# Optimization experiments

Hardware: AMD Instinct MI355X
Metric: run time of the kernel (lower is better)

## Reference

```python
import jax, jax.numpy as jnp
import numpy as np

# ---- config (matches init_kwargs) ----
GROUP_NUM = 2048
K_NEIGHBORS = 32
OUT_DIM = 192
SIGMA, BASELINE, SCALING, EPS = 0.26, 0.1, 10.0, 1e-6
ALPHA, BETA = 1000.0, 100.0
ADAPTIVE_RATIO = 0.5
IN_DIM = 3
ADAPTIVE_DIM = int(OUT_DIM * ADAPTIVE_RATIO)          # 96
FOURIER_DIM = OUT_DIM - ADAPTIVE_DIM                  # 96
FEAT_DIM_F = FOURIER_DIM // (IN_DIM * 2)              # 16
FEAT_DIM_A = int(np.ceil(ADAPTIVE_DIM / IN_DIM))      # 32
FEAT_NUM_A = FEAT_DIM_A * IN_DIM                      # 96
OUT_IDX = np.linspace(0, FEAT_NUM_A - 1, ADAPTIVE_DIM).astype(np.int64)


def setup_inputs() -> dict:
    key = jax.random.key(0)
    k1, k2, k3, k4 = jax.random.split(key, 4)
    xyz = jax.random.normal(k1, (4, 8192, 3), dtype=jnp.float32)
    x = jax.random.normal(k2, (4, 8192, 96), dtype=jnp.float32)
    bn_gamma = jax.random.uniform(k3, (192,), dtype=jnp.float32)
    bn_beta = jax.random.normal(k4, (192,), dtype=jnp.float32)
    return {"xyz": xyz, "x": x, "bn_gamma": bn_gamma, "bn_beta": bn_beta}


def _fps(xyz, m):
    """Farthest point sampling. xyz: [B,N,3] -> idx [B,m] (int32). Seed = index 0."""
    def single(pts):
        n = pts.shape[0]
        def step(carry, _):
            dists, last = carry
            d = jnp.sum((pts - pts[last]) ** 2, axis=-1)
            dists = jnp.minimum(dists, d)
            nxt = jnp.argmax(dists).astype(jnp.int32)
            return (dists, nxt), nxt
        init = (jnp.full((n,), 1e10, pts.dtype), jnp.array(0, jnp.int32))
        _, idxs = jax.lax.scan(step, init, None, length=m - 1)
        return jnp.concatenate([jnp.zeros((1,), jnp.int32), idxs])
    return jax.vmap(single)(xyz)


def _square_distance(src, dst):
    # src: [B,S,3], dst: [B,N,3] -> [B,S,N]
    d = -2.0 * jnp.einsum('bsc,bnc->bsn', src, dst)
    d += jnp.sum(src ** 2, -1)[:, :, None]
    d += jnp.sum(dst ** 2, -1)[:, None, :]
    return d


def _gather_knn(points, idx):
    # points: [B,N,C], idx: [B,G,K] -> [B,G,K,C]
    return jax.vmap(lambda p, i: p[i])(points, idx)


def _forward(xyz, x, bn_gamma, bn_beta):
    B, N, _ = xyz.shape
    G, K = GROUP_NUM, K_NEIGHBORS

    # ---- Grouper_seg ----
    fps_idx = _fps(xyz, G)                                   # [B,G]
    lc_xyz = jnp.take_along_axis(xyz, fps_idx[..., None], 1)  # [B,G,3]
    lc_x = jnp.take_along_axis(x, fps_idx[..., None], 1)      # [B,G,C]
    sqr = _square_distance(lc_xyz, xyz)                       # [B,G,N]
    knn_idx = jax.lax.top_k(-sqr, K)[1]                       # [B,G,K] smallest-k
    knn_xyz = _gather_knn(xyz, knn_idx)                       # [B,G,K,3]
    knn_x = _gather_knn(x, knn_idx)                           # [B,G,K,C]

    # ---- Aggregation_seg: local normalization ----
    mean_x = lc_x[:, :, None, :]
    std_x = jnp.std(knn_x - mean_x, ddof=1)
    mean_xyz = lc_xyz[:, :, None, :]
    std_xyz = jnp.std(knn_xyz - mean_xyz, ddof=1)
    knn_x = (knn_x - mean_x) / (std_x + 1e-5)
    knn_xyz_n = (knn_xyz - mean_xyz) / (std_xyz + 1e-5)       # [B,G,K,3]
    C = knn_x.shape[-1]
    knn_x = jnp.concatenate(
        [knn_x, jnp.broadcast_to(lc_x[:, :, None, :], (B, G, K, C))], axis=-1)  # [B,G,K,2C]
    knn_xyz_cf = jnp.transpose(knn_xyz_n, (0, 3, 1, 2))       # [B,3,G,K]
    knn_x_cf = jnp.transpose(knn_x, (0, 3, 1, 2))             # [B,OUT_DIM,G,K]

    # ---- PosE_Geo: fourier part ----
    feat_range = jnp.arange(FEAT_DIM_F, dtype=knn_xyz_cf.dtype)
    dim_embed = ALPHA ** (feat_range / FEAT_DIM_F)            # [F]
    div = BETA * knn_xyz_cf[..., None] / dim_embed            # [B,3,G,K,F]
    fourier = jnp.stack([jnp.sin(div), jnp.cos(div)], axis=-1)  # [B,3,G,K,F,2]
    fourier = fourier.reshape(B, IN_DIM, G, K, 2 * FEAT_DIM_F)
    fourier = jnp.transpose(fourier, (0, 1, 4, 2, 3)).reshape(B, FOURIER_DIM, G, K)

    # ---- AdaptiveEmbedding (parameterless, data-driven) ----
    x4 = knn_xyz_n                                            # [B,G,K,3]
    gstd = jnp.mean(jnp.std(x4.reshape(B, -1, IN_DIM), axis=1, ddof=1))
    sig = SIGMA * (1.0 + gstd) + EPS
    blend = jax.nn.sigmoid((gstd - BASELINE) * SCALING)
    feat_val = jnp.linspace(-1.0, 1.0, FEAT_DIM_A + 2)[1:-1]  # [Fa]
    z = (x4[..., None] - feat_val) / sig                      # [B,G,K,3,Fa]
    comb = blend * jnp.exp(-0.5 * z * z) + (1.0 - blend) * jnp.cos(z)
    ae = comb.reshape(B, G, K, FEAT_NUM_A)[..., OUT_IDX]      # [B,G,K,ADAPTIVE_DIM]
    ae_cf = jnp.transpose(ae, (0, 3, 1, 2))                   # [B,ADAPTIVE_DIM,G,K]

    pe = jnp.concatenate([fourier, ae_cf], axis=1)            # [B,OUT_DIM,G,K]
    knn_x_w = (knn_x_cf + pe) * pe

    # ---- Pooling_seg: max+mean pool, BatchNorm1d (train stats) + GELU ----
    lc = jnp.max(knn_x_w, -1) + jnp.mean(knn_x_w, -1)         # [B,OUT_DIM,G]
    mu = jnp.mean(lc, axis=(0, 2), keepdims=True)
    var = jnp.var(lc, axis=(0, 2), keepdims=True)
    y = (lc - mu) / jnp.sqrt(var + 1e-5)
    y = y * bn_gamma[None, :, None] + bn_beta[None, :, None]
    return jax.nn.gelu(y, approximate=False)


def reference(xyz, x, bn_gamma, bn_beta):
    return _forward(xyz, x, bn_gamma, bn_beta)
```

## Files before the change

kernel.cpp:

```cpp
#include <hip/hip_runtime.h>
#include <cstdint>
#include <math.h>

#define NPTS 8192
#define NB 4
#define NG 2048
#define NK 32
#define CIN 96
#define COUT 192

typedef float v2f __attribute__((ext_vector_type(2)));
typedef unsigned long long ull;

__global__ __launch_bounds__(256) void setup_kernel(const float* __restrict__ xyz,
                                                    float* __restrict__ xs, float* __restrict__ ys,
                                                    float* __restrict__ zs, float* __restrict__ d2){
  int i = blockIdx.x*256 + threadIdx.x;
  if (i >= NB*NPTS) return;
  float x = xyz[3*i+0], y = xyz[3*i+1], z = xyz[3*i+2];
  xs[i]=x; ys[i]=y; zs[i]=z;
  d2[i] = __fadd_rn(__fadd_rn(__fmul_rn(x,x),__fmul_rn(y,y)),__fmul_rn(z,z));
}

template<int CTRL>
__device__ __forceinline__ float dppmaxf(float v){
  int o = __builtin_amdgcn_update_dpp(__float_as_int(v), __float_as_int(v), CTRL, 0xf, 0xf, false);
  return fmaxf(v, __int_as_float(o));
}
template<int CTRL>
__device__ __forceinline__ unsigned dppminu(unsigned v){
  unsigned o = (unsigned)__builtin_amdgcn_update_dpp((int)v, (int)v, CTRL, 0xf, 0xf, false);
  return (o < v) ? o : v;
}
__device__ __forceinline__ float wavemaxf(float v){
  v = dppmaxf<0x111>(v); v = dppmaxf<0x112>(v); v = dppmaxf<0x114>(v);
  v = dppmaxf<0x118>(v); v = dppmaxf<0x142>(v); v = dppmaxf<0x143>(v);
  return v;
}
__device__ __forceinline__ unsigned waveminu(unsigned v){
  v = dppminu<0x111>(v); v = dppminu<0x112>(v); v = dppminu<0x114>(v);
  v = dppminu<0x118>(v); v = dppminu<0x142>(v); v = dppminu<0x143>(v);
  return v;
}

__global__ __launch_bounds__(512,2) void fps_kernel(const float* __restrict__ xyz, int* __restrict__ fps_idx){
#pragma clang fp contract(off)
  extern __shared__ char smem[];
  float4* ctab = (float4*)smem;
  ull* wavekeys = (ull*)(smem + NPTS*16);
  const int b = blockIdx.x;
  const int t = threadIdx.x;
  const int w = t>>6, lane = t&63;
  const float* base = xyz + (size_t)b*NPTS*3;
  v2f px[8], py[8], pz[8], D[8];
#pragma unroll
  for (int j=0;j<8;++j){
    int p0 = t + 1024*j, p1 = p0 + 512;
    float x0=base[3*p0+0], y0=base[3*p0+1], z0=base[3*p0+2];
    float x1=base[3*p1+0], y1=base[3*p1+1], z1=base[3*p1+2];
    px[j]=(v2f){x0,x1}; py[j]=(v2f){y0,y1}; pz[j]=(v2f){z0,z1};
    D[j]=(v2f){1e10f,1e10f};
    ctab[p0] = make_float4(x0,y0,z0,0.f);
    ctab[p1] = make_float4(x1,y1,z1,0.f);
  }
  if (t==0) fps_idx[b*NG]=0;
  __syncthreads();
  float lx=base[0], ly=base[1], lz=base[2];
  for (int it=0; it<NG-1; ++it){
    v2f bm = (v2f){-1.0f,-1.0f};
#pragma unroll
    for (int j=0;j<8;++j){
      v2f dx = px[j]-lx, dy = py[j]-ly, dz = pz[j]-lz;
      v2f s = (dx*dx + dy*dy) + dz*dz;
      v2f nd = __builtin_elementwise_min(D[j], s);
      D[j] = nd;
      bm = __builtin_elementwise_max(bm, nd);
    }
    float bd = fmaxf(bm.x, bm.y);
    float m = wavemaxf(bd);
    float bdw = __int_as_float(__builtin_amdgcn_readlane(__float_as_int(m), 63));
    unsigned li = 0xFFFFFFFFu;
    if (bd == bdw){
#pragma unroll
      for (int j=7;j>=0;--j){
        if (D[j].y == bdw) li = (unsigned)(t + (j<<10) + 512);
        if (D[j].x == bdw) li = (unsigned)(t + (j<<10));
      }
    }
    unsigned mn = waveminu(li);
    if (lane==63)
      wavekeys[(it&1)*8 + w] = (((ull)__float_as_uint(bdw))<<32) | (ull)(~mn);
    __syncthreads();
    const ull* wk = wavekeys + (it&1)*8;
    ull k = wk[0];
#pragma unroll
    for (int q=1;q<8;++q){ ull o = wk[q]; if (o > k) k = o; }
    unsigned pw = ~(unsigned)k;
    float4 c = ctab[pw];
    lx=c.x; ly=c.y; lz=c.z;
    if (t==0) fps_idx[b*NG + it + 1] = (int)pw;
  }
}

__device__ __forceinline__ bool lexlt(float ad, int ai, float bd, int bi){
  return (ad < bd) || ((ad == bd) && (ai < bi));
}
__device__ __forceinline__ void sort_desc(float& d, int& i, int lane){
#pragma unroll
  for (int k=2;k<=64;k<<=1){
#pragma unroll
    for (int j=k>>1;j>0;j>>=1){
      float od = __shfl_xor(d, j);
      int   oi = __shfl_xor(i, j);
      bool dirUp = (lane & k) != 0;
      bool lower = (lane & j) == 0;
      bool less  = lexlt(d,i,od,oi);
      bool keep  = (less == (lower == dirUp));
      if (!keep){ d=od; i=oi; }
    }
  }
}
__device__ __forceinline__ void merge_asc(float& d, int& i, int lane){
#pragma unroll
  for (int j=32;j>0;j>>=1){
    float od = __shfl_xor(d, j);
    int   oi = __shfl_xor(i, j);
    bool lower = (lane & j) == 0;
    bool less  = lexlt(d,i,od,oi);
    bool keep  = (less == lower);
    if (!keep){ d=od; i=oi; }
  }
}

__global__ __launch_bounds__(256) void knn_kernel(const float* __restrict__ xs, const float* __restrict__ ys,
                                                  const float* __restrict__ zs, const float* __restrict__ d2,
                                                  const int* __restrict__ fps_idx, int* __restrict__ knn_out){
  __shared__ float tx[256], ty[256], tz[256], td[256];
  const int tid = threadIdx.x;
  const int wid = tid>>6, lane = tid&63;
  const int pid = blockIdx.x*4 + wid;
  const int b = pid >> 11;
  const float* bx = xs + b*NPTS;
  const float* by = ys + b*NPTS;
  const float* bz = zs + b*NPTS;
  const float* bD = d2 + b*NPTS;
  const int fi = fps_idx[pid];
  const float ax = bx[fi], ay = by[fi], az = bz[fi];
  const float src2 = __fadd_rn(__fadd_rn(__fmul_rn(ax,ax),__fmul_rn(ay,ay)),__fmul_rn(az,az));
  float Ad = INFINITY; int Ai = 0x7fffffff;
  float tau_d = INFINITY; int tau_i = 0x7fffffff;
  for (int s=0; s<NPTS/256; ++s){
    __syncthreads();
    int gidx = s*256 + tid;
    tx[tid]=bx[gidx]; ty[tid]=by[gidx]; tz[tid]=bz[gidx]; td[tid]=bD[gidx];
    __syncthreads();
    float m0,m1,m2,m3; int i0,i1,i2,i3;
#define LOADJ(mj, ij, J) { int li = (J)*64 + lane; \
    float dot = __fadd_rn(__fadd_rn(__fmul_rn(ax,tx[li]),__fmul_rn(ay,ty[li])),__fmul_rn(az,tz[li])); \
    mj = __fadd_rn(__fadd_rn(__fmul_rn(-2.0f,dot), src2), td[li]); ij = s*256 + li; }
    LOADJ(m0,i0,0) LOADJ(m1,i1,1) LOADJ(m2,i2,2) LOADJ(m3,i3,3)
#undef LOADJ
    while (true){
      bool any = lexlt(m0,i0,tau_d,tau_i) || lexlt(m1,i1,tau_d,tau_i) ||
                 lexlt(m2,i2,tau_d,tau_i) || lexlt(m3,i3,tau_d,tau_i);
      if (__ballot(any) == 0ull) break;
      float cd = m0; int ci = i0; int sel = 0;
      if (lexlt(m1,i1,cd,ci)){ cd=m1; ci=i1; sel=1; }
      if (lexlt(m2,i2,cd,ci)){ cd=m2; ci=i2; sel=2; }
      if (lexlt(m3,i3,cd,ci)){ cd=m3; ci=i3; sel=3; }
      if      (sel==0) m0=INFINITY;
      else if (sel==1) m1=INFINITY;
      else if (sel==2) m2=INFINITY;
      else             m3=INFINITY;
      sort_desc(cd, ci, lane);
      if (lexlt(cd,ci,Ad,Ai)){ Ad=cd; Ai=ci; }
      merge_asc(Ad, Ai, lane);
      tau_d = __shfl(Ad, 31);
      tau_i = __shfl(Ai, 31);
    }
  }
  if (lane < NK) knn_out[pid*NK + lane] = Ai;
}

__global__ __launch_bounds__(256) void stats_kernel(const float* __restrict__ x, const float* __restrict__ xyz,
                                                    const int* __restrict__ fps_idx, const int* __restrict__ knn,
                                                    double* __restrict__ partials){
  const int tid=threadIdx.x, wid=tid>>6, lane=tid&63;
  const int pid = blockIdx.x*4 + wid;
  const int b = pid>>11;
  const int fi = fps_idx[pid];
  const float* xb = x + (size_t)b*NPTS*CIN;
  const float* zb = xyz + (size_t)b*NPTS*3;
  const float lc0 = xb[fi*CIN + lane];
  float lc1 = 0.f; if (lane<32) lc1 = xb[fi*CIN + 64 + lane];
  float czv = 0.f; if (lane<3)  czv = zb[fi*3 + lane];
  double s1=0.0, s2=0.0, a1=0.0, a2=0.0;
  for (int k=0;k<NK;++k){
    int idx = knn[pid*NK + k];
    float d0 = __fsub_rn(xb[idx*CIN + lane], lc0);
    s1 += (double)d0; s2 += (double)d0*(double)d0;
    if (lane<32){
      float d1 = __fsub_rn(xb[idx*CIN + 64 + lane], lc1);
      s1 += (double)d1; s2 += (double)d1*(double)d1;
    }
    if (lane<3){
      float w = __fsub_rn(zb[idx*3 + lane], czv);
      a1 += (double)w; a2 += (double)w*(double)w;
    }
  }
#pragma unroll
  for (int off=32; off>0; off>>=1){ s1 += __shfl_xor(s1,off); s2 += __shfl_xor(s2,off); }
  __shared__ double shx[4][2];
  __shared__ double shz[4][3][2];
  if (lane==0){ shx[wid][0]=s1; shx[wid][1]=s2; }
  if (lane<3){ shz[wid][lane][0]=a1; shz[wid][lane][1]=a2; }
  __syncthreads();
  if (tid==0){
    double u0=0,u1=0;
    for (int w=0;w<4;++w){ u0+=shx[w][0]; u1+=shx[w][1]; }
    double* outp = partials + (size_t)blockIdx.x*8;
    outp[0]=u0; outp[1]=u1;
    for (int axq=0; axq<3; ++axq){
      double v0=0,v1=0;
      for (int w=0;w<4;++w){ v0+=shz[w][axq][0]; v1+=shz[w][axq][1]; }
      outp[2+2*axq]=v0; outp[3+2*axq]=v1;
    }
  }
}

__global__ void finalize_kernel(const double* __restrict__ partials, float* __restrict__ scal){
  const int lane = threadIdx.x;
  double s1=0,s2=0;
  double z0a=0,z0b=0,z1a=0,z1b=0,z2a=0,z2b=0;
  for (int i=0;i<32;++i){
    const double* p = partials + (size_t)(lane*32+i)*8;
    s1+=p[0]; s2+=p[1];
    z0a+=p[2]; z0b+=p[3]; z1a+=p[4]; z1b+=p[5]; z2a+=p[6]; z2b+=p[7];
  }
#pragma unroll
  for (int off=32; off>0; off>>=1){ s1+=__shfl_xor(s1,off); s2+=__shfl_xor(s2,off); }
#pragma unroll
  for (int off=8; off>0; off>>=1){
    z0a+=__shfl_xor(z0a,off); z0b+=__shfl_xor(z0b,off);
    z1a+=__shfl_xor(z1a,off); z1b+=__shfl_xor(z1b,off);
    z2a+=__shfl_xor(z2a,off); z2b+=__shfl_xor(z2b,off);
  }
  __shared__ double zb[4][3][2];
  if ((lane&15)==0){
    int b = lane>>4;
    zb[b][0][0]=z0a; zb[b][0][1]=z0b;
    zb[b][1][0]=z1a; zb[b][1][1]=z1b;
    zb[b][2][0]=z2a; zb[b][2][1]=z2b;
  }
  __syncthreads();
  if (lane==0){
    double nx = (double)NB*NG*NK*CIN;
    double varx = (s2 - s1*s1/nx)/(nx-1.0);
    float stdx = (float)sqrt(varx);
    double t1=0,t2=0;
    for (int b=0;b<4;++b) for (int a=0;a<3;++a){ t1+=zb[b][a][0]; t2+=zb[b][a][1]; }
    double nz = (double)NB*NG*NK*3;
    double varz = (t2 - t1*t1/nz)/(nz-1.0);
    float stdz = (float)sqrt(varz);
    float sdiv = stdz + 1e-5f;
    double n2 = (double)NG*NK;
    double acc=0.0;
    for (int b=0;b<4;++b) for (int a=0;a<3;++a){
      double v = (zb[b][a][1] - zb[b][a][0]*zb[b][a][0]/n2)/(n2-1.0);
      acc += sqrt(v);
    }
    float gstd = (float)(acc/12.0) / sdiv;
    float sig = 0.26f*(1.0f+gstd) + 1e-6f;
    float blend = 1.0f/(1.0f + expf(-(gstd-0.1f)*10.0f));
    scal[0] = 1.0f/(stdx + 1e-5f);
    scal[1] = 1.0f/sdiv;
    scal[2] = 1.0f/sig;
    scal[3] = blend;
  }
}

__global__ __launch_bounds__(256) void main_kernel(const float* __restrict__ x, const float* __restrict__ xyz,
                                                   const int* __restrict__ fps_idx, const int* __restrict__ knn,
                                                   const float* __restrict__ scal, float* __restrict__ lc_out){
  const int tid=threadIdx.x, wid=tid>>6, lane=tid&63;
  const int pid = blockIdx.x*4 + wid;
  const int b = pid>>11, g = pid&2047;
  const float inv_x = scal[0], inv_z = scal[1], inv_sig = scal[2], blend = scal[3];
  const float omb = 1.0f - blend;
  const int fi = fps_idx[pid];
  const float* xb = x + (size_t)b*NPTS*CIN;
  const float* zb = xyz + (size_t)b*NPTS*3;
  const float cx = zb[fi*3+0], cy = zb[fi*3+1], cz = zb[fi*3+2];
  const float lcx0 = xb[fi*CIN + lane];
  const float lcx1 = (lane<32) ? xb[fi*CIN + 64 + lane] : xb[fi*CIN + lane - 32];
  const float lcx2 = xb[fi*CIN + 32 + lane];
  const int dim0 = lane>>5;
  const int rr0 = lane&31;
  const bool cos0 = rr0 & 1;
  const float bs0 = 100.0f / powf(1000.0f, (float)(rr0>>1) * (1.0f/16.0f));
  const bool cos1 = lane & 1;
  const float bs1 = 100.0f / powf(1000.0f, (float)((lane&31)>>1) * (1.0f/16.0f));
  const float fv1 = (float)(-1.0 + 2.0*(double)(lane-32+1)/33.0);
  const int dim2 = (32+lane)>>5;
  const int j2 = (32+lane)&31;
  const float fv2 = (float)(-1.0 + 2.0*(double)(j2+1)/33.0);

  float mx0=-INFINITY, mx1=-INFINITY, mx2=-INFINITY;
  float sm0=0.f, sm1=0.f, sm2=0.f;
  for (int k=0;k<NK;++k){
    const int idx = knn[pid*NK + k];
    const float p0 = zb[idx*3+0], p1 = zb[idx*3+1], p2v = zb[idx*3+2];
    const float xn0 = (p0-cx)*inv_z, xn1 = (p1-cy)*inv_z, xn2 = (p2v-cz)*inv_z;
    const float xk0 = xb[idx*CIN + lane];
    float xk1 = 0.f; if (lane<32) xk1 = xb[idx*CIN + 64 + lane];
    {
      float v = dim0 ? xn1 : xn0;
      float a = v * bs0;
      float pe = cos0 ? __cosf(a) : __sinf(a);
      float f = (xk0 - lcx0) * inv_x;
      float w = (f + pe) * pe;
      mx0 = fmaxf(mx0, w); sm0 += w;
    }
    {
      float pe, f;
      if (lane < 32){
        float a = xn2 * bs1;
        pe = cos1 ? __cosf(a) : __sinf(a);
        f = (xk1 - lcx1) * inv_x;
      } else {
        float zq = (xn0 - fv1) * inv_sig;
        pe = blend * __expf(-0.5f*zq*zq) + omb * __cosf(zq);
        f = lcx1;
      }
      float w = (f + pe) * pe;
      mx1 = fmaxf(mx1, w); sm1 += w;
    }
    {
      float v = (dim2==1) ? xn1 : xn2;
      float zq = (v - fv2) * inv_sig;
      float pe = blend * __expf(-0.5f*zq*zq) + omb * __cosf(zq);
      float w = (lcx2 + pe) * pe;
      mx2 = fmaxf(mx2, w); sm2 += w;
    }
  }
  const size_t obase = ((size_t)b*COUT)*NG + g;
  lc_out[obase + (size_t)lane*NG]       = mx0 + sm0*(1.0f/32.0f);
  lc_out[obase + (size_t)(64+lane)*NG]  = mx1 + sm1*(1.0f/32.0f);
  lc_out[obase + (size_t)(128+lane)*NG] = mx2 + sm2*(1.0f/32.0f);
}

__global__ __launch_bounds__(256) void bn_stats_kernel(const float* __restrict__ lc, float* __restrict__ bn){
  const int c = blockIdx.x, t = threadIdx.x, lane=t&63, wid=t>>6;
  double s1=0.0, s2=0.0;
  for (int i=t; i<NB*NG; i+=256){
    int b=i>>11, g=i&2047;
    float v = lc[((size_t)(b*COUT)+c)*NG + g];
    s1 += (double)v; s2 += (double)v*(double)v;
  }
#pragma unroll
  for (int off=32; off>0; off>>=1){ s1+=__shfl_xor(s1,off); s2+=__shfl_xor(s2,off); }
  __shared__ double sh1[4], sh2[4];
  if (lane==0){ sh1[wid]=s1; sh2[wid]=s2; }
  __syncthreads();
  if (t==0){
    double a=sh1[0]+sh1[1]+sh1[2]+sh1[3], q=sh2[0]+sh2[1]+sh2[2]+sh2[3];
    double n=(double)(NB*NG);
    double mu=a/n, var=q/n - mu*mu;
    bn[c]=(float)mu;
    bn[COUT+c]=(float)(1.0/sqrt(var + 1e-5));
  }
}

__global__ __launch_bounds__(256) void final_kernel(const float* __restrict__ bn, const float* __restrict__ gamma,
                                                    const float* __restrict__ beta, float* __restrict__ out){
  int i = blockIdx.x*256 + threadIdx.x;
  int c = (i >> 11) % COUT;
  float v = out[i];
  float y = (v - bn[c]) * bn[COUT + c];
  y = y*gamma[c] + beta[c];
  out[i] = y * 0.5f * (1.0f + erff(y * 0.70710678118654752f));
}

extern "C" void kernel_launch(void* const* d_in, const int* in_sizes, int n_in,
                              void* d_out, int out_size, void* d_ws, size_t ws_size,
                              hipStream_t stream){
  const float* xyz   = (const float*)d_in[0];
  const float* x     = (const float*)d_in[1];
  const float* gamma = (const float*)d_in[2];
  const float* beta  = (const float*)d_in[3];
  float* out = (float*)d_out;
  char* ws = (char*)d_ws;
  int*    fps  = (int*)   (ws + 0);
  int*    knn  = (int*)   (ws + 32768);
  float*  xs   = (float*) (ws + 1081344);
  float*  ys   = (float*) (ws + 1212416);
  float*  zs   = (float*) (ws + 1343488);
  float*  d2   = (float*) (ws + 1474560);
  double* parts= (double*)(ws + 1605632);
  float*  scal = (float*) (ws + 1736704);
  float*  bn   = (float*) (ws + 1736768);

  const int fps_lds = NPTS*16 + 2*8*8;
  (void)hipFuncSetAttribute(reinterpret_cast<const void*>(fps_kernel),
                            hipFuncAttributeMaxDynamicSharedMemorySize, fps_lds);

  setup_kernel   <<<dim3((NB*NPTS+255)/256), dim3(256), 0, stream>>>(xyz, xs, ys, zs, d2);
  fps_kernel     <<<dim3(NB),                dim3(512), fps_lds, stream>>>(xyz, fps);
  knn_kernel     <<<dim3(NB*NG/4),           dim3(256), 0, stream>>>(xs, ys, zs, d2, fps, knn);
  stats_kernel   <<<dim3(NB*NG/4),           dim3(256), 0, stream>>>(x, xyz, fps, knn, parts);
  finalize_kernel<<<dim3(1),                 dim3(64),  0, stream>>>(parts, scal);
  main_kernel    <<<dim3(NB*NG/4),           dim3(256), 0, stream>>>(x, xyz, fps, knn, scal, out);
  bn_stats_kernel<<<dim3(COUT),              dim3(256), 0, stream>>>(out, bn);
  final_kernel   <<<dim3((NB*COUT*NG)/256),  dim3(256), 0, stream>>>(bn, gamma, beta, out);
}
```

Measured before the change: 2.555 ms.

## Spatially sort FPS points per wave and skip waves via bounding-box bound

Reorders the points of each batch in the FPS kernel into Morton-ordered 8x8x8 cells, using a shared-memory histogram and scatter, so that each wave owns a spatially compact chunk with its own bounding box. At every iteration a wave computes a lower bound on the distance from the new centroid to its box. If that bound exceeds the wave's current max of min-distances, the wave skips the distance update and republishes its cached key. This is meant to remove most of the per-iteration distance work in the sequential FPS loop. The cost is setup work, extra registers (16 points per thread) and a key encoding that keeps the lowest-original-index tie-break.

```diff
diff --git a/kernel.cpp b/kernel.cpp
--- a/kernel.cpp
+++ b/kernel.cpp
@@ -9,7 +9,6 @@
 #define CIN 96
 #define COUT 192
 
-typedef float v2f __attribute__((ext_vector_type(2)));
 typedef unsigned long long ull;
 
 __global__ __launch_bounds__(256) void setup_kernel(const float* __restrict__ xyz,
@@ -28,18 +27,18 @@
   return fmaxf(v, __int_as_float(o));
 }
 template<int CTRL>
-__device__ __forceinline__ unsigned dppminu(unsigned v){
+__device__ __forceinline__ unsigned dppmaxu(unsigned v){
   unsigned o = (unsigned)__builtin_amdgcn_update_dpp((int)v, (int)v, CTRL, 0xf, 0xf, false);
-  return (o < v) ? o : v;
+  return (o > v) ? o : v;
 }
 __device__ __forceinline__ float wavemaxf(float v){
   v = dppmaxf<0x111>(v); v = dppmaxf<0x112>(v); v = dppmaxf<0x114>(v);
   v = dppmaxf<0x118>(v); v = dppmaxf<0x142>(v); v = dppmaxf<0x143>(v);
   return v;
 }
-__device__ __forceinline__ unsigned waveminu(unsigned v){
-  v = dppminu<0x111>(v); v = dppminu<0x112>(v); v = dppminu<0x114>(v);
-  v = dppminu<0x118>(v); v = dppminu<0x142>(v); v = dppminu<0x143>(v);
+__device__ __forceinline__ unsigned wavemaxu(unsigned v){
+  v = dppmaxu<0x111>(v); v = dppmaxu<0x112>(v); v = dppmaxu<0x114>(v);
+  v = dppmaxu<0x118>(v); v = dppmaxu<0x142>(v); v = dppmaxu<0x143>(v);
   return v;
 }
 
@@ -47,58 +46,141 @@
 #pragma clang fp contract(off)
   extern __shared__ char smem[];
   float4* ctab = (float4*)smem;
-  ull* wavekeys = (ull*)(smem + NPTS*16);
-  const int b = blockIdx.x;
-  const int t = threadIdx.x;
+  ull*    keys = (ull*)(smem + 131072);
+  int*    hist = (int*)(smem + 131072 + 128);
+  float*  bbs  = (float*)(smem + 131072 + 128 + 2048);
+  const int b = blockIdx.x, t = threadIdx.x;
   const int w = t>>6, lane = t&63;
   const float* base = xyz + (size_t)b*NPTS*3;
-  v2f px[8], py[8], pz[8], D[8];
-#pragma unroll
-  for (int j=0;j<8;++j){
-    int p0 = t + 1024*j, p1 = p0 + 512;
-    float x0=base[3*p0+0], y0=base[3*p0+1], z0=base[3*p0+2];
-    float x1=base[3*p1+0], y1=base[3*p1+1], z1=base[3*p1+2];
-    px[j]=(v2f){x0,x1}; py[j]=(v2f){y0,y1}; pz[j]=(v2f){z0,z1};
-    D[j]=(v2f){1e10f,1e10f};
-    ctab[p0] = make_float4(x0,y0,z0,0.f);
-    ctab[p1] = make_float4(x1,y1,z1,0.f);
-  }
-  if (t==0) fps_idx[b*NG]=0;
-  __syncthreads();
+
+  float ox[16], oy[16], oz[16];
+#pragma unroll
+  for (int j=0;j<16;++j){
+    int p = t + 512*j;
+    ox[j]=base[3*p+0]; oy[j]=base[3*p+1]; oz[j]=base[3*p+2];
+  }
+  float mnx=ox[0],mxx=ox[0],mny=oy[0],mxy=oy[0],mnz=oz[0],mxz=oz[0];
+#pragma unroll
+  for (int j=1;j<16;++j){
+    mnx=fminf(mnx,ox[j]); mxx=fmaxf(mxx,ox[j]);
+    mny=fminf(mny,oy[j]); mxy=fmaxf(mxy,oy[j]);
+    mnz=fminf(mnz,oz[j]); mxz=fmaxf(mxz,oz[j]);
+  }
+#pragma unroll
+  for (int off=32; off>0; off>>=1){
+    mnx=fminf(mnx,__shfl_xor(mnx,off)); mxx=fmaxf(mxx,__shfl_xor(mxx,off));
+    mny=fminf(mny,__shfl_xor(mny,off)); mxy=fmaxf(mxy,__shfl_xor(mxy,off));
+    mnz=fminf(mnz,__shfl_xor(mnz,off)); mxz=fmaxf(mxz,__shfl_xor(mxz,off));
+  }
+  hist[t] = 0;
+  if (lane==0){
+    bbs[w*6+0]=mnx; bbs[w*6+1]=mxx; bbs[w*6+2]=mny;
+    bbs[w*6+3]=mxy; bbs[w*6+4]=mnz; bbs[w*6+5]=mxz;
+  }
+  if (t==0) fps_idx[b*NG] = 0;
+  __syncthreads();
+  float gx0=1e30f,gx1=-1e30f,gy0=1e30f,gy1=-1e30f,gz0=1e30f,gz1=-1e30f;
+  for (int q=0;q<8;++q){
+    gx0=fminf(gx0,bbs[q*6+0]); gx1=fmaxf(gx1,bbs[q*6+1]);
+    gy0=fminf(gy0,bbs[q*6+2]); gy1=fmaxf(gy1,bbs[q*6+3]);
+    gz0=fminf(gz0,bbs[q*6+4]); gz1=fmaxf(gz1,bbs[q*6+5]);
+  }
+  const float sxv = 8.0f/fmaxf(gx1-gx0,1e-20f);
+  const float syv = 8.0f/fmaxf(gy1-gy0,1e-20f);
+  const float szv = 8.0f/fmaxf(gz1-gz0,1e-20f);
+  int cell[16];
+#pragma unroll
+  for (int j=0;j<16;++j){
+    int cx = min(7,(int)((ox[j]-gx0)*sxv));
+    int cy = min(7,(int)((oy[j]-gy0)*syv));
+    int cz = min(7,(int)((oz[j]-gz0)*szv));
+    int m = (cx&1) | ((cy&1)<<1) | ((cz&1)<<2)
+          | ((cx&2)<<2) | ((cy&2)<<3) | ((cz&2)<<4)
+          | ((cx&4)<<4) | ((cy&4)<<5) | ((cz&4)<<6);
+    cell[j]=m;
+    atomicAdd(&hist[m],1);
+  }
+  __syncthreads();
+  if (t==0){
+    int run=0;
+    for (int c=0;c<512;++c){ int h=hist[c]; hist[c]=run; run+=h; }
+  }
+  __syncthreads();
+#pragma unroll
+  for (int j=0;j<16;++j){
+    int pos = atomicAdd(&hist[cell[j]],1);
+    ctab[pos] = make_float4(ox[j],oy[j],oz[j], __int_as_float(t+512*j));
+  }
+  __syncthreads();
+  float px[16],py[16],pz[16],D[16]; unsigned lowb[16];
+  float bx0,bx1,by0,by1,bz0,bz1;
+#pragma unroll
+  for (int j=0;j<16;++j){
+    int pos = (w<<10) + (j<<6) + lane;
+    float4 c4 = ctab[pos];
+    px[j]=c4.x; py[j]=c4.y; pz[j]=c4.z;
+    unsigned orig = (unsigned)__float_as_int(c4.w);
+    lowb[j] = ((8191u-orig)<<13) | (unsigned)pos;
+    D[j] = 1e10f;
+    if (j==0){ bx0=c4.x; bx1=c4.x; by0=c4.y; by1=c4.y; bz0=c4.z; bz1=c4.z; }
+    else {
+      bx0=fminf(bx0,c4.x); bx1=fmaxf(bx1,c4.x);
+      by0=fminf(by0,c4.y); by1=fmaxf(by1,c4.y);
+      bz0=fminf(bz0,c4.z); bz1=fmaxf(bz1,c4.z);
+    }
+  }
+#pragma unroll
+  for (int off=32; off>0; off>>=1){
+    bx0=fminf(bx0,__shfl_xor(bx0,off)); bx1=fmaxf(bx1,__shfl_xor(bx1,off));
+    by0=fminf(by0,__shfl_xor(by0,off)); by1=fmaxf(by1,__shfl_xor(by1,off));
+    bz0=fminf(bz0,__shfl_xor(bz0,off)); bz1=fmaxf(bz1,__shfl_xor(bz1,off));
+  }
+
   float lx=base[0], ly=base[1], lz=base[2];
+  float Mw = 1e10f;
+  unsigned mylow = 0;
   for (int it=0; it<NG-1; ++it){
-    v2f bm = (v2f){-1.0f,-1.0f};
-#pragma unroll
-    for (int j=0;j<8;++j){
-      v2f dx = px[j]-lx, dy = py[j]-ly, dz = pz[j]-lz;
-      v2f s = (dx*dx + dy*dy) + dz*dz;
-      v2f nd = __builtin_elementwise_min(D[j], s);
-      D[j] = nd;
-      bm = __builtin_elementwise_max(bm, nd);
-    }
-    float bd = fmaxf(bm.x, bm.y);
-    float m = wavemaxf(bd);
-    float bdw = __int_as_float(__builtin_amdgcn_readlane(__float_as_int(m), 63));
-    unsigned li = 0xFFFFFFFFu;
-    if (bd == bdw){
-#pragma unroll
-      for (int j=7;j>=0;--j){
-        if (D[j].y == bdw) li = (unsigned)(t + (j<<10) + 512);
-        if (D[j].x == bdw) li = (unsigned)(t + (j<<10));
+    float qx=fminf(fmaxf(lx,bx0),bx1);
+    float qy=fminf(fmaxf(ly,by0),by1);
+    float qz=fminf(fmaxf(lz,bz0),bz1);
+    float ddx=qx-lx, ddy=qy-ly, ddz=qz-lz;
+    float LB = (ddx*ddx+ddy*ddy)+ddz*ddz;
+    ull* kslot = &keys[(it&1)*8 + w];
+    if (LB <= Mw*1.0001f){
+      float bd=-1.0f;
+#pragma unroll
+      for (int j=0;j<16;++j){
+        float dx=px[j]-lx, dy=py[j]-ly, dz=pz[j]-lz;
+        float d=(dx*dx+dy*dy)+dz*dz;
+        float nd=fminf(D[j],d);
+        D[j]=nd;
+        bd=fmaxf(bd,nd);
       }
-    }
-    unsigned mn = waveminu(li);
-    if (lane==63)
-      wavekeys[(it&1)*8 + w] = (((ull)__float_as_uint(bdw))<<32) | (ull)(~mn);
+      unsigned bl=0;
+#pragma unroll
+      for (int j=0;j<16;++j){
+        unsigned c2 = (lowb[j]>bl)?lowb[j]:bl;
+        bl = (D[j]==bd) ? c2 : bl;
+      }
+      float m = wavemaxf(bd);
+      float bdw = __int_as_float(__builtin_amdgcn_readlane(__float_as_int(m),63));
+      unsigned cand = (bd==bdw) ? bl : 0u;
+      unsigned mu = wavemaxu(cand);
+      if (lane==63) *kslot = (((ull)__float_as_uint(bdw))<<32) | (ull)mu;
+      Mw = bdw;
+      mylow = (unsigned)__builtin_amdgcn_readlane((int)mu,63);
+    } else {
+      if (lane==63) *kslot = (((ull)__float_as_uint(Mw))<<32) | (ull)mylow;
+    }
     __syncthreads();
-    const ull* wk = wavekeys + (it&1)*8;
-    ull k = wk[0];
-#pragma unroll
-    for (int q=1;q<8;++q){ ull o = wk[q]; if (o > k) k = o; }
-    unsigned pw = ~(unsigned)k;
-    float4 c = ctab[pw];
-    lx=c.x; ly=c.y; lz=c.z;
-    if (t==0) fps_idx[b*NG + it + 1] = (int)pw;
+    const ull* kk = keys + (it&1)*8;
+    ull k = kk[0];
+#pragma unroll
+    for (int q=1;q<8;++q){ ull o=kk[q]; if (o>k) k=o; }
+    unsigned lw = (unsigned)k;
+    float4 c4 = ctab[lw & 0x1FFFu];
+    lx=c4.x; ly=c4.y; lz=c4.z;
+    if (t==0) fps_idx[b*NG + it + 1] = (int)(8191u - ((lw>>13)&0x1FFFu));
   }
 }
 
@@ -400,7 +482,7 @@
   float*  scal = (float*) (ws + 1736704);
   float*  bn   = (float*) (ws + 1736768);
 
-  const int fps_lds = NPTS*16 + 2*8*8;
+  const int fps_lds = 131072 + 128 + 2048 + 192;
   (void)hipFuncSetAttribute(reinterpret_cast<const void*>(fps_kernel),
                             hipFuncAttributeMaxDynamicSharedMemorySize, fps_lds);
 
```

Measured after the change: 2.433 ms. 4.8% less time.
